# Kernel optimization log

Measured on AMD Instinct MI355X. Metric: run time of the kernel, lower is better.

## Reference

```python
import jax, jax.numpy as jnp
import numpy as np

B, S, DM, H, HD = 2, 4096, 768, 12, 64
SCALING = HD ** -0.5
LN_EPS = 1e-12
ROPE_BASE = 10000.0


def rotate_half(x):
    x1, x2 = jnp.split(x, 2, axis=-1)
    return jnp.concatenate([-x2, x1], axis=-1)


def setup_inputs() -> dict:
    key = jax.random.key(0)
    ks = jax.random.split(key, 8)
    s = 0.02
    hidden_states = jax.random.normal(ks[0], (B, S, DM), dtype=jnp.float32)
    # true rotary tables: inv_freq over head_dim/2, duplicated (HF convention)
    inv_freq = 1.0 / (ROPE_BASE ** (jnp.arange(0, HD, 2, dtype=jnp.float32) / HD))
    freqs = jnp.arange(S, dtype=jnp.float32)[:, None] * inv_freq[None, :]  # [S, HD/2]
    emb = jnp.concatenate([freqs, freqs], axis=-1)                          # [S, HD]
    cos, sin = jnp.cos(emb), jnp.sin(emb)
    return {
        "hidden_states": hidden_states,
        "cos": cos,
        "sin": sin,
        "Wq": jax.random.normal(ks[1], (DM, DM), dtype=jnp.float32) * s,
        "bq": jnp.zeros((DM,), dtype=jnp.float32),
        "Wk": jax.random.normal(ks[2], (DM, DM), dtype=jnp.float32) * s,
        "bk": jnp.zeros((DM,), dtype=jnp.float32),
        "Wv": jax.random.normal(ks[3], (DM, DM), dtype=jnp.float32) * s,
        "bv": jnp.zeros((DM,), dtype=jnp.float32),
        "Wo": jax.random.normal(ks[4], (DM, DM), dtype=jnp.float32) * s,
        "ln_g": jnp.ones((DM,), dtype=jnp.float32),
        "ln_b": jnp.zeros((DM,), dtype=jnp.float32),
    }


def reference(hidden_states, cos, sin, Wq, bq, Wk, bk, Wv, bv, Wo, ln_g, ln_b):
    # QKV projections -> [B, H, S, HD]
    def proj(W, b):
        return (hidden_states @ W.T + b).reshape(B, S, H, HD).transpose(0, 2, 1, 3)
    q, k, v = proj(Wq, bq), proj(Wk, bk), proj(Wv, bv)

    # RoPE (cos/sin broadcast over batch & heads)
    c = cos[None, None, :, :]
    s_ = sin[None, None, :, :]
    q = q * c + rotate_half(q) * s_
    k = k * c + rotate_half(k) * s_

    # Faithful to source: q pre-scaled, then eager attention scales scores again
    q = q * SCALING
    scores = jnp.einsum("bhsd,bhtd->bhst", q, k) * SCALING  # [B,H,S,S]
    probs = jax.nn.softmax(scores.astype(jnp.float32), axis=-1).astype(v.dtype)
    attn = jnp.einsum("bhst,bhtd->bhsd", probs, v)
    attn = attn.transpose(0, 2, 1, 3).reshape(B, S, DM)

    # output dense (no bias) + residual + LayerNorm
    out = attn @ Wo.T + hidden_states
    mu = jnp.mean(out, axis=-1, keepdims=True)
    var = jnp.var(out, axis=-1, keepdims=True)
    out = (out - mu) * jax.lax.rsqrt(var + LN_EPS) * ln_g + ln_b
    return out
```

## Files before the change

kernel.cpp:

```cpp
#include <hip/hip_runtime.h>
#include <math.h>

#define B_   2
#define S_   4096
#define DM_  768
#define H_   12
#define HD_  64
#define M_   (B_ * S_)
#define ROWELEMS ((size_t)M_ * DM_)
#define WELEMS  ((size_t)DM_ * DM_)

#define QSC (1.4426950408889634f / 64.0f)

typedef unsigned short u16;
typedef unsigned int   u32;
typedef __attribute__((ext_vector_type(8))) short  short8;
typedef __attribute__((ext_vector_type(4))) float  floatx4;

__device__ inline u16 f2bf(float f) {
    u32 u = __builtin_bit_cast(u32, f);
    u += 0x7FFF + ((u >> 16) & 1);
    return (u16)(u >> 16);
}
__device__ inline float bf2f(u16 h) {
    return __builtin_bit_cast(float, (u32)h << 16);
}
__device__ inline u32 pk_trunc(float a, float b) {
    return __builtin_amdgcn_perm(__builtin_bit_cast(u32, b),
                                 __builtin_bit_cast(u32, a), 0x07060302);
}

__device__ inline int sw_off(int r, int cg) {
    return (r << 6) + ((cg ^ (r & 7)) << 3);
}

__device__ __forceinline__ void load_lds16(const u16* g, u16* l) {
    __builtin_amdgcn_global_load_lds(
        (const __attribute__((address_space(1))) u32*)g,
        (__attribute__((address_space(3))) u32*)l, 16, 0, 0);
}

__global__ __launch_bounds__(256) void conv_bf16(
    const float* __restrict__ h,  const float* __restrict__ wq,
    const float* __restrict__ wk, const float* __restrict__ wv,
    const float* __restrict__ wo, u16* __restrict__ hb, u16* __restrict__ wb)
{
    const int y = blockIdx.y;
    const float* src; u16* dst; size_t n4;
    if (y == 0)      { src = h;  dst = hb;              n4 = ROWELEMS / 4; }
    else if (y == 1) { src = wq; dst = wb;              n4 = WELEMS / 4; }
    else if (y == 2) { src = wk; dst = wb + WELEMS;     n4 = WELEMS / 4; }
    else if (y == 3) { src = wv; dst = wb + 2 * WELEMS; n4 = WELEMS / 4; }
    else             { src = wo; dst = wb + 3 * WELEMS; n4 = WELEMS / 4; }
    const size_t stride = (size_t)gridDim.x * 256;
    for (size_t i = blockIdx.x * 256 + threadIdx.x; i < n4; i += stride) {
        float4 v = *(const float4*)&src[i * 4];
        u32 p0 = (u32)f2bf(v.x) | ((u32)f2bf(v.y) << 16);
        u32 p1 = (u32)f2bf(v.z) | ((u32)f2bf(v.w) << 16);
        *(uint2*)&dst[i * 4] = make_uint2(p0, p1);
    }
}

__global__ __launch_bounds__(256, 3) void gemm_qkv(
    const u16* __restrict__ A,
    const u16* __restrict__ W0, const u16* __restrict__ W1, const u16* __restrict__ W2,
    const float* __restrict__ b0, const float* __restrict__ b1, const float* __restrict__ b2,
    const float* __restrict__ cosT, const float* __restrict__ sinT,
    u16* __restrict__ Qh, u16* __restrict__ Kh, u16* __restrict__ Vt)
{
    __shared__ __align__(16) u16 As[128 * 64];
    __shared__ __align__(16) u16 Ws[128 * 64];

    const int tid  = threadIdx.x;
    const int wave = tid >> 6, lane = tid & 63;
    const int n16  = lane & 15, quad = lane >> 4;
    const int wm   = wave >> 1, wn = wave & 1;
    const int m0   = blockIdx.y * 128, n0 = blockIdx.x * 128;
    const int z    = blockIdx.z;

    const u16* Wz = (z == 0) ? W0 : (z == 1) ? W1 : W2;
    const float* bz = (z == 0) ? b0 : (z == 1) ? b1 : b2;

    int gao[4], ldso[4];
#pragma unroll
    for (int i = 0; i < 4; i++) {
        int g = wave * 256 + i * 64 + lane;
        int r = g >> 3, cg = (g & 7) ^ (r & 7);
        gao[i]  = r * DM_ + cg * 8;
        ldso[i] = (wave * 256 + i * 64) * 8;
    }
    const u16* Ap = A  + (size_t)m0 * DM_;
    const u16* Wp = Wz + (size_t)n0 * DM_;

    floatx4 acc[4][4];
#pragma unroll
    for (int i = 0; i < 4; i++)
#pragma unroll
        for (int j = 0; j < 4; j++) acc[i][j] = (floatx4){0.f, 0.f, 0.f, 0.f};

    for (int k0 = 0; k0 < DM_; k0 += 64) {
        __syncthreads();
#pragma unroll
        for (int i = 0; i < 4; i++) {
            load_lds16(Ap + k0 + gao[i], &As[ldso[i]]);
            load_lds16(Wp + k0 + gao[i], &Ws[ldso[i]]);
        }
        __syncthreads();
#pragma unroll
        for (int ks = 0; ks < 2; ks++) {
            short8 af[4], bf[4];
#pragma unroll
            for (int t = 0; t < 4; t++) {
                af[t] = *(const short8*)&As[sw_off(wm * 64 + t * 16 + n16, ks * 4 + quad)];
                bf[t] = *(const short8*)&Ws[sw_off(wn * 64 + t * 16 + n16, ks * 4 + quad)];
            }
#pragma unroll
            for (int i = 0; i < 4; i++)
#pragma unroll
                for (int j = 0; j < 4; j++)
                    acc[i][j] = __builtin_amdgcn_mfma_f32_16x16x32_bf16(
                        af[i], bf[j], acc[i][j], 0, 0, 0);
        }
    }

    if (z == 2) {
#pragma unroll
        for (int i = 0; i < 4; i++)
#pragma unroll
            for (int j = 0; j < 4; j++) {
                const int col = n0 + wn * 64 + j * 16 + n16;
                const int h = col >> 6, hd = col & 63;
                const int row0 = m0 + wm * 64 + i * 16 + quad * 4;
                const int b = row0 >> 12, s0 = row0 & 4095;
                const float bias = bz[col];
                float v0 = acc[i][j][0] + bias, v1 = acc[i][j][1] + bias;
                float v2 = acc[i][j][2] + bias, v3 = acc[i][j][3] + bias;
                u32 w0 = (u32)f2bf(v0) | ((u32)f2bf(v1) << 16);
                u32 w1 = (u32)f2bf(v2) | ((u32)f2bf(v3) << 16);
                *(uint2*)&Vt[((size_t)(b * H_ + h) * HD_ + hd) * S_ + s0] = make_uint2(w0, w1);
            }
    } else {
        u16* Out = (z == 0) ? Qh : Kh;
        const float sc_ = (z == 0) ? QSC : 1.0f;
#pragma unroll
        for (int i = 0; i < 4; i++)
#pragma unroll
            for (int j = 0; j < 2; j++) {
                const int col1 = n0 + wn * 64 + j * 16 + n16;
                const int col2 = col1 + 32;
                const int h = col1 >> 6, hd1 = col1 & 63;
                const float bias1 = bz[col1], bias2 = bz[col2];
#pragma unroll
                for (int r = 0; r < 4; r++) {
                    const int row = m0 + wm * 64 + i * 16 + quad * 4 + r;
                    const int b = row >> 12, s = row & 4095;
                    const float c  = cosT[s * HD_ + hd1];
                    const float sn = sinT[s * HD_ + hd1];
                    const float x1 = acc[i][j][r] + bias1;
                    const float x2 = acc[i][j + 2][r] + bias2;
                    u16* dst = Out + ((size_t)(b * H_ + h) * S_ + s) * HD_;
                    dst[hd1]      = f2bf((x1 * c - x2 * sn) * sc_);
                    dst[hd1 + 32] = f2bf((x2 * c + x1 * sn) * sc_);
                }
            }
    }
}

__global__ __launch_bounds__(256, 4) void flash_mfma(
    const u16* __restrict__ Qh, const u16* __restrict__ Kh,
    const u16* __restrict__ Vt, u16* __restrict__ O1, u16* __restrict__ O2,
    float* __restrict__ l1, float* __restrict__ l2)
{
    __shared__ __align__(16) u16 Ks[64 * 64];
    __shared__ __align__(16) u16 Vs[64 * 64];
    __shared__ __align__(16) u16 Ps[128 * 64];

    const int tid  = threadIdx.x;
    const int wave = tid >> 6, lane = tid & 63;
    const int n16  = lane & 15, quad = lane >> 4;
    const int qt   = blockIdx.x;
    const int bh   = blockIdx.y;
    const int z    = blockIdx.z;
    const size_t qk_base = (size_t)bh * S_ * HD_;
    const size_t vt_base = (size_t)bh * HD_ * S_;
    const int q0   = qt * 128;
    const int wrow = wave * 32;

    short8 qf[2][2];
#pragma unroll
    for (int rt = 0; rt < 2; rt++)
#pragma unroll
        for (int ks = 0; ks < 2; ks++)
            qf[rt][ks] = *(const short8*)&Qh[qk_base +
                (size_t)(q0 + wrow + rt * 16 + n16) * HD_ + ks * 32 + quad * 8];

    int gk_off[2], gv_off[2], ldso[2];
#pragma unroll
    for (int i = 0; i < 2; i++) {
        int g = wave * 128 + i * 64 + lane;
        int r = g >> 3, cg = (g & 7) ^ (r & 7);
        gk_off[i] = r * HD_ + cg * 8;
        gv_off[i] = r * S_  + cg * 8;
        ldso[i]   = (wave * 128 + i * 64) * 8;
    }

    floatx4 o_acc[2][4];
    float l_part[2] = {0.0f, 0.0f};
#pragma unroll
    for (int rt = 0; rt < 2; rt++)
#pragma unroll
        for (int dt = 0; dt < 4; dt++) o_acc[rt][dt] = (floatx4){0.f, 0.f, 0.f, 0.f};

    const u16* Kg = Kh + qk_base + (size_t)(z * 32) * 64 * HD_;
    const u16* Vg = Vt + vt_base + (size_t)(z * 32) * 64;

    for (int kt = 0; kt < 32; kt++) {
        __syncthreads();
#pragma unroll
        for (int i = 0; i < 2; i++) {
            load_lds16(Kg + gk_off[i], &Ks[ldso[i]]);
            load_lds16(Vg + gv_off[i], &Vs[ldso[i]]);
        }
        __syncthreads();
        Kg += 64 * HD_;
        Vg += 64;

        floatx4 sct[4][2];
#pragma unroll
        for (int ct = 0; ct < 4; ct++)
#pragma unroll
            for (int rt = 0; rt < 2; rt++)
                sct[ct][rt] = (floatx4){0.f, 0.f, 0.f, 0.f};
#pragma unroll
        for (int ks = 0; ks < 2; ks++) {
            short8 kf[4];
#pragma unroll
            for (int ct = 0; ct < 4; ct++)
                kf[ct] = *(const short8*)&Ks[sw_off(ct * 16 + n16, ks * 4 + quad)];
#pragma unroll
            for (int ct = 0; ct < 4; ct++)
#pragma unroll
                for (int rt = 0; rt < 2; rt++)
                    sct[ct][rt] = __builtin_amdgcn_mfma_f32_16x16x32_bf16(
                        kf[ct], qf[rt][ks], sct[ct][rt], 0, 0, 0);
        }

#pragma unroll
        for (int rt = 0; rt < 2; rt++)
#pragma unroll
            for (int ct = 0; ct < 4; ct++) {
                float p0 = __builtin_amdgcn_exp2f(sct[ct][rt][0]);
                float p1 = __builtin_amdgcn_exp2f(sct[ct][rt][1]);
                float p2 = __builtin_amdgcn_exp2f(sct[ct][rt][2]);
                float p3 = __builtin_amdgcn_exp2f(sct[ct][rt][3]);
                l_part[rt] += (p0 + p1) + (p2 + p3);
                uint2 w = make_uint2(pk_trunc(p0, p1), pk_trunc(p2, p3));
                const int row = wrow + rt * 16 + n16;
                const int off = sw_off(row, ct * 2 + (quad >> 1)) + (quad & 1) * 4;
                *(uint2*)&Ps[off] = w;
            }

#pragma unroll
        for (int ks = 0; ks < 2; ks++) {
            short8 pa[2];
#pragma unroll
            for (int rt = 0; rt < 2; rt++)
                pa[rt] = *(const short8*)&Ps[sw_off(wrow + rt * 16 + n16, ks * 4 + quad)];
            short8 vb[4];
#pragma unroll
            for (int dt = 0; dt < 4; dt++)
                vb[dt] = *(const short8*)&Vs[sw_off(dt * 16 + n16, ks * 4 + quad)];
#pragma unroll
            for (int rt = 0; rt < 2; rt++)
#pragma unroll
                for (int dt = 0; dt < 4; dt++)
                    o_acc[rt][dt] = __builtin_amdgcn_mfma_f32_16x16x32_bf16(
                        pa[rt], vb[dt], o_acc[rt][dt], 0, 0, 0);
        }
    }

    float* lz = z ? l2 : l1;
#pragma unroll
    for (int rt = 0; rt < 2; rt++) {
        float v = l_part[rt];
        v += __shfl_xor(v, 16);
        v += __shfl_xor(v, 32);
        if (lane < 16)
            lz[(size_t)bh * S_ + q0 + wrow + rt * 16 + lane] = v;
    }
    const int b = bh / H_, h = bh % H_;
    u16* Oz = z ? O2 : O1;
#pragma unroll
    for (int rt = 0; rt < 2; rt++)
#pragma unroll
        for (int r = 0; r < 4; r++) {
            const int srow = q0 + wrow + rt * 16 + quad * 4 + r;
            u16* Orow = Oz + ((size_t)b * S_ + srow) * DM_ + h * HD_;
#pragma unroll
            for (int dt = 0; dt < 4; dt++)
                Orow[dt * 16 + n16] = f2bf(o_acc[rt][dt][r]);
        }
}

__global__ __launch_bounds__(256, 4) void gemm_out(
    const u16* __restrict__ O1, const u16* __restrict__ O2,
    const float* __restrict__ l1, const float* __restrict__ l2,
    const u16* __restrict__ W, const float* __restrict__ resid,
    float* __restrict__ Cf)
{
    __shared__ __align__(16) u16 As[64 * 64];
    __shared__ __align__(16) u16 Ws[128 * 64];

    const int tid  = threadIdx.x;
    const int wave = tid >> 6, lane = tid & 63;
    const int n16  = lane & 15, quad = lane >> 4;
    const int wm   = wave >> 1, wn = wave & 1;
    const int m0   = blockIdx.y * 64, n0 = blockIdx.x * 128;

    int gwo[4], ldswo[4];
#pragma unroll
    for (int i = 0; i < 4; i++) {
        int g = wave * 256 + i * 64 + lane;
        int r = g >> 3, cg = (g & 7) ^ (r & 7);
        gwo[i]   = r * DM_ + cg * 8;
        ldswo[i] = (wave * 256 + i * 64) * 8;
    }
    const u16* Wp = W + (size_t)n0 * DM_;

    floatx4 acc[2][4];
#pragma unroll
    for (int i = 0; i < 2; i++)
#pragma unroll
        for (int j = 0; j < 4; j++) acc[i][j] = (floatx4){0.f, 0.f, 0.f, 0.f};

    for (int k0 = 0; k0 < DM_; k0 += 64) {
        __syncthreads();
#pragma unroll
        for (int i = 0; i < 4; i++)
            load_lds16(Wp + k0 + gwo[i], &Ws[ldswo[i]]);

#pragma unroll
        for (int i = 0; i < 2; i++) {
            const int ga = tid + i * 256;
            const int ra = ga >> 3, cga = ga & 7;
            const int row = m0 + ra;
            const int col0 = k0 + cga * 8;
            const int b = row >> 12, s = row & 4095, h = col0 >> 6;
            const size_t lidx = ((size_t)(b * H_ + h)) * S_ + s;
            const float inv = __builtin_amdgcn_rcpf(l1[lidx] + l2[lidx]);
            const size_t go = (size_t)row * DM_ + col0;
            uint4 a = *(const uint4*)&O1[go];
            uint4 c = *(const uint4*)&O2[go];
            u32 res[4];
#pragma unroll
            for (int w = 0; w < 4; w++) {
                u32 ua = (&a.x)[w], uc = (&c.x)[w];
                float x0 = bf2f((u16)(ua & 0xFFFF)) + bf2f((u16)(uc & 0xFFFF));
                float x1 = bf2f((u16)(ua >> 16))    + bf2f((u16)(uc >> 16));
                res[w] = (u32)f2bf(x0 * inv) | ((u32)f2bf(x1 * inv) << 16);
            }
            *(uint4*)&As[sw_off(ra, cga)] = make_uint4(res[0], res[1], res[2], res[3]);
        }
        __syncthreads();

#pragma unroll
        for (int ks = 0; ks < 2; ks++) {
            short8 af[2], bf[4];
#pragma unroll
            for (int rt = 0; rt < 2; rt++)
                af[rt] = *(const short8*)&As[sw_off(wm * 32 + rt * 16 + n16, ks * 4 + quad)];
#pragma unroll
            for (int ct = 0; ct < 4; ct++)
                bf[ct] = *(const short8*)&Ws[sw_off(wn * 64 + ct * 16 + n16, ks * 4 + quad)];
#pragma unroll
            for (int rt = 0; rt < 2; rt++)
#pragma unroll
                for (int ct = 0; ct < 4; ct++)
                    acc[rt][ct] = __builtin_amdgcn_mfma_f32_16x16x32_bf16(
                        af[rt], bf[ct], acc[rt][ct], 0, 0, 0);
        }
    }

#pragma unroll
    for (int rt = 0; rt < 2; rt++)
#pragma unroll
        for (int ct = 0; ct < 4; ct++) {
            const int col = n0 + wn * 64 + ct * 16 + n16;
#pragma unroll
            for (int r = 0; r < 4; r++) {
                const int row = m0 + wm * 32 + rt * 16 + quad * 4 + r;
                Cf[(size_t)row * DM_ + col] = acc[rt][ct][r] + resid[(size_t)row * DM_ + col];
            }
        }
}

__global__ __launch_bounds__(256) void ln_kernel(
    float* __restrict__ io, const float* __restrict__ g, const float* __restrict__ bb)
{
    const int row = blockIdx.x, t = threadIdx.x;
    float* p = io + (size_t)row * DM_;
    float x[3];
    float sum = 0.0f, sq = 0.0f;
#pragma unroll
    for (int i = 0; i < 3; i++) {
        x[i] = p[t + i * 256];
        sum += x[i];
        sq  = fmaf(x[i], x[i], sq);
    }
#pragma unroll
    for (int off = 32; off >= 1; off >>= 1) {
        sum += __shfl_xor(sum, off);
        sq  += __shfl_xor(sq, off);
    }
    __shared__ float s1[4], s2[4];
    if ((t & 63) == 0) { s1[t >> 6] = sum; s2[t >> 6] = sq; }
    __syncthreads();
    sum = s1[0] + s1[1] + s1[2] + s1[3];
    sq  = s2[0] + s2[1] + s2[2] + s2[3];
    const float mu  = sum * (1.0f / 768.0f);
    const float var = sq * (1.0f / 768.0f) - mu * mu;
    const float rs  = rsqrtf(var + 1e-12f);
#pragma unroll
    for (int i = 0; i < 3; i++) {
        const int c = t + i * 256;
        p[c] = (x[i] - mu) * rs * g[c] + bb[c];
    }
}

extern "C" void kernel_launch(void* const* d_in, const int* in_sizes, int n_in,
                              void* d_out, int out_size, void* d_ws, size_t ws_size,
                              hipStream_t stream)
{
    const float* hidden = (const float*)d_in[0];
    const float* cosT   = (const float*)d_in[1];
    const float* sinT   = (const float*)d_in[2];
    const float* Wq     = (const float*)d_in[3];
    const float* bq     = (const float*)d_in[4];
    const float* Wk     = (const float*)d_in[5];
    const float* bk     = (const float*)d_in[6];
    const float* Wv     = (const float*)d_in[7];
    const float* bv     = (const float*)d_in[8];
    const float* Wo     = (const float*)d_in[9];
    const float* ln_g   = (const float*)d_in[10];
    const float* ln_b   = (const float*)d_in[11];
    float* out = (float*)d_out;

    u16* wsb = (u16*)d_ws;
    u16* Hb  = wsb;
    u16* Wb  = wsb + ROWELEMS;
    u16* Qh  = Wb + 4 * WELEMS;
    u16* Kh  = Qh + ROWELEMS;
    u16* Vt  = Kh + ROWELEMS;
    u16* O2  = Vt + ROWELEMS;
    float* l1 = (float*)(O2 + ROWELEMS);
    float* l2 = l1 + (size_t)B_ * H_ * S_;
    u16* O1  = Hb;
    u16* Wqb = Wb, *Wkb = Wb + WELEMS, *Wvb = Wb + 2 * WELEMS, *Wob = Wb + 3 * WELEMS;

    conv_bf16<<<dim3(1024, 5), 256, 0, stream>>>(hidden, Wq, Wk, Wv, Wo, Hb, Wb);

    gemm_qkv<<<dim3(DM_ / 128, M_ / 128, 3), 256, 0, stream>>>(
        Hb, Wqb, Wkb, Wvb, bq, bk, bv, cosT, sinT, Qh, Kh, Vt);

    flash_mfma<<<dim3(S_ / 128, B_ * H_, 2), 256, 0, stream>>>(
        Qh, Kh, Vt, O1, O2, l1, l2);

    gemm_out<<<dim3(DM_ / 128, M_ / 64), 256, 0, stream>>>(
        O1, O2, l1, l2, Wob, hidden, out);

    ln_kernel<<<M_, 256, 0, stream>>>(out, ln_g, ln_b);
}
```

Measured before the change: 300.9 us.

## Double-buffer K/V tiles in flash kernel and compute row sums via MFMA

The flash attention kernel now double-buffers K and V tiles in LDS. It prefetches the next tile while computing on the current one and drops one of the two barriers per iteration. The softmax denominator is now computed with an extra MFMA against a ones vector on the bf16-truncated probabilities, replacing the scalar accumulation and shuffle reduction. Launch bounds drop to 3 blocks per SM to fit the larger LDS footprint. The single barrier plus waitcnt ordering, and computing the sum from truncated P, could introduce races or small numeric differences.

```diff
diff --git a/kernel.cpp b/kernel.cpp
--- a/kernel.cpp
+++ b/kernel.cpp
@@ -166,13 +166,13 @@
     }
 }
 
-__global__ __launch_bounds__(256, 4) void flash_mfma(
+__global__ __launch_bounds__(256, 3) void flash_mfma(
     const u16* __restrict__ Qh, const u16* __restrict__ Kh,
     const u16* __restrict__ Vt, u16* __restrict__ O1, u16* __restrict__ O2,
     float* __restrict__ l1, float* __restrict__ l2)
 {
-    __shared__ __align__(16) u16 Ks[64 * 64];
-    __shared__ __align__(16) u16 Vs[64 * 64];
+    __shared__ __align__(16) u16 Ks[2][64 * 64];
+    __shared__ __align__(16) u16 Vs[2][64 * 64];
     __shared__ __align__(16) u16 Ps[128 * 64];
 
     const int tid  = threadIdx.x;
@@ -194,6 +194,10 @@
             qf[rt][ks] = *(const short8*)&Qh[qk_base +
                 (size_t)(q0 + wrow + rt * 16 + n16) * HD_ + ks * 32 + quad * 8];
 
+    short8 ones;
+#pragma unroll
+    for (int j = 0; j < 8; j++) ones[j] = (short)0x3F80;
+
     int gk_off[2], gv_off[2], ldso[2];
 #pragma unroll
     for (int i = 0; i < 2; i++) {
@@ -205,25 +209,38 @@
     }
 
     floatx4 o_acc[2][4];
-    float l_part[2] = {0.0f, 0.0f};
-#pragma unroll
-    for (int rt = 0; rt < 2; rt++)
+    floatx4 o_l[2];
+#pragma unroll
+    for (int rt = 0; rt < 2; rt++) {
+        o_l[rt] = (floatx4){0.f, 0.f, 0.f, 0.f};
 #pragma unroll
         for (int dt = 0; dt < 4; dt++) o_acc[rt][dt] = (floatx4){0.f, 0.f, 0.f, 0.f};
-
-    const u16* Kg = Kh + qk_base + (size_t)(z * 32) * 64 * HD_;
-    const u16* Vg = Vt + vt_base + (size_t)(z * 32) * 64;
+    }
+
+    const u16* Kg0 = Kh + qk_base + (size_t)(z * 32) * 64 * HD_;
+    const u16* Vg0 = Vt + vt_base + (size_t)(z * 32) * 64;
+
+#pragma unroll
+    for (int i = 0; i < 2; i++) {
+        load_lds16(Kg0 + gk_off[i], &Ks[0][ldso[i]]);
+        load_lds16(Vg0 + gv_off[i], &Vs[0][ldso[i]]);
+    }
 
     for (int kt = 0; kt < 32; kt++) {
+        const int cur = kt & 1, nxt = cur ^ 1;
         __syncthreads();
-#pragma unroll
-        for (int i = 0; i < 2; i++) {
-            load_lds16(Kg + gk_off[i], &Ks[ldso[i]]);
-            load_lds16(Vg + gv_off[i], &Vs[ldso[i]]);
-        }
-        __syncthreads();
-        Kg += 64 * HD_;
-        Vg += 64;
+
+        {
+            const int ktn = (kt < 31) ? kt + 1 : 31;
+            const u16* Kg = Kg0 + (size_t)ktn * 64 * HD_;
+            const u16* Vg = Vg0 + (size_t)ktn * 64;
+#pragma unroll
+            for (int i = 0; i < 2; i++) {
+                load_lds16(Kg + gk_off[i], &Ks[nxt][ldso[i]]);
+                load_lds16(Vg + gv_off[i], &Vs[nxt][ldso[i]]);
+            }
+        }
+        __builtin_amdgcn_s_waitcnt(0x0F74);
 
         floatx4 sct[4][2];
 #pragma unroll
@@ -236,7 +253,7 @@
             short8 kf[4];
 #pragma unroll
             for (int ct = 0; ct < 4; ct++)
-                kf[ct] = *(const short8*)&Ks[sw_off(ct * 16 + n16, ks * 4 + quad)];
+                kf[ct] = *(const short8*)&Ks[cur][sw_off(ct * 16 + n16, ks * 4 + quad)];
 #pragma unroll
             for (int ct = 0; ct < 4; ct++)
 #pragma unroll
@@ -253,7 +270,6 @@
                 float p1 = __builtin_amdgcn_exp2f(sct[ct][rt][1]);
                 float p2 = __builtin_amdgcn_exp2f(sct[ct][rt][2]);
                 float p3 = __builtin_amdgcn_exp2f(sct[ct][rt][3]);
-                l_part[rt] += (p0 + p1) + (p2 + p3);
                 uint2 w = make_uint2(pk_trunc(p0, p1), pk_trunc(p2, p3));
                 const int row = wrow + rt * 16 + n16;
                 const int off = sw_off(row, ct * 2 + (quad >> 1)) + (quad & 1) * 4;
@@ -269,24 +285,26 @@
             short8 vb[4];
 #pragma unroll
             for (int dt = 0; dt < 4; dt++)
-                vb[dt] = *(const short8*)&Vs[sw_off(dt * 16 + n16, ks * 4 + quad)];
-#pragma unroll
-            for (int rt = 0; rt < 2; rt++)
+                vb[dt] = *(const short8*)&Vs[cur][sw_off(dt * 16 + n16, ks * 4 + quad)];
+#pragma unroll
+            for (int rt = 0; rt < 2; rt++) {
 #pragma unroll
                 for (int dt = 0; dt < 4; dt++)
                     o_acc[rt][dt] = __builtin_amdgcn_mfma_f32_16x16x32_bf16(
                         pa[rt], vb[dt], o_acc[rt][dt], 0, 0, 0);
+                o_l[rt] = __builtin_amdgcn_mfma_f32_16x16x32_bf16(
+                    pa[rt], ones, o_l[rt], 0, 0, 0);
+            }
         }
     }
 
     float* lz = z ? l2 : l1;
-#pragma unroll
-    for (int rt = 0; rt < 2; rt++) {
-        float v = l_part[rt];
-        v += __shfl_xor(v, 16);
-        v += __shfl_xor(v, 32);
-        if (lane < 16)
-            lz[(size_t)bh * S_ + q0 + wrow + rt * 16 + lane] = v;
+    if (n16 == 0) {
+#pragma unroll
+        for (int rt = 0; rt < 2; rt++)
+#pragma unroll
+            for (int r = 0; r < 4; r++)
+                lz[(size_t)bh * S_ + q0 + wrow + rt * 16 + quad * 4 + r] = o_l[rt][r];
     }
     const int b = bh / H_, h = bh % H_;
     u16* Oz = z ? O2 : O1;
```

Result: no change. 299.0 us (-0.6%).

## Double query rows per flash block to reuse K/V tiles across more rows

Applied to the files above, without the earlier changes.

Each flash attention block now covers 256 query rows instead of 128, with each wave owning 64 rows, so every K/V tile staged in shared memory serves twice as many queries. QK^T and the exp/pack step are restructured to loop per 16-row tile, with K fragments loaded once per tile, which keeps the live score registers small. The aim is to halve global K/V traffic and the number of syncthreads per unit of work. In exchange, register and LDS use per block go up (launch bounds drop to 3 blocks per CU) and the grid halves to 768 blocks.

```diff
diff --git a/kernel.cpp b/kernel.cpp
--- a/kernel.cpp
+++ b/kernel.cpp
@@ -166,14 +166,14 @@
     }
 }
 
-__global__ __launch_bounds__(256, 4) void flash_mfma(
+__global__ __launch_bounds__(256, 3) void flash_mfma(
     const u16* __restrict__ Qh, const u16* __restrict__ Kh,
     const u16* __restrict__ Vt, u16* __restrict__ O1, u16* __restrict__ O2,
     float* __restrict__ l1, float* __restrict__ l2)
 {
     __shared__ __align__(16) u16 Ks[64 * 64];
     __shared__ __align__(16) u16 Vs[64 * 64];
-    __shared__ __align__(16) u16 Ps[128 * 64];
+    __shared__ __align__(16) u16 Ps[256 * 64];
 
     const int tid  = threadIdx.x;
     const int wave = tid >> 6, lane = tid & 63;
@@ -183,12 +183,12 @@
     const int z    = blockIdx.z;
     const size_t qk_base = (size_t)bh * S_ * HD_;
     const size_t vt_base = (size_t)bh * HD_ * S_;
-    const int q0   = qt * 128;
-    const int wrow = wave * 32;
-
-    short8 qf[2][2];
-#pragma unroll
-    for (int rt = 0; rt < 2; rt++)
+    const int q0   = qt * 256;
+    const int wrow = wave * 64;
+
+    short8 qf[4][2];
+#pragma unroll
+    for (int rt = 0; rt < 4; rt++)
 #pragma unroll
         for (int ks = 0; ks < 2; ks++)
             qf[rt][ks] = *(const short8*)&Qh[qk_base +
@@ -204,84 +204,79 @@
         ldso[i]   = (wave * 128 + i * 64) * 8;
     }
 
-    floatx4 o_acc[2][4];
-    float l_part[2] = {0.0f, 0.0f};
-#pragma unroll
-    for (int rt = 0; rt < 2; rt++)
+    floatx4 o_acc[4][4];
+    float l_part[4] = {0.f, 0.f, 0.f, 0.f};
+#pragma unroll
+    for (int rt = 0; rt < 4; rt++)
 #pragma unroll
         for (int dt = 0; dt < 4; dt++) o_acc[rt][dt] = (floatx4){0.f, 0.f, 0.f, 0.f};
 
-    const u16* Kg = Kh + qk_base + (size_t)(z * 32) * 64 * HD_;
-    const u16* Vg = Vt + vt_base + (size_t)(z * 32) * 64;
+    const u16* Kg0 = Kh + qk_base + (size_t)(z * 32) * 64 * HD_;
+    const u16* Vg0 = Vt + vt_base + (size_t)(z * 32) * 64;
 
     for (int kt = 0; kt < 32; kt++) {
         __syncthreads();
 #pragma unroll
         for (int i = 0; i < 2; i++) {
-            load_lds16(Kg + gk_off[i], &Ks[ldso[i]]);
-            load_lds16(Vg + gv_off[i], &Vs[ldso[i]]);
-        }
-        __syncthreads();
-        Kg += 64 * HD_;
-        Vg += 64;
-
-        floatx4 sct[4][2];
-#pragma unroll
-        for (int ct = 0; ct < 4; ct++)
-#pragma unroll
-            for (int rt = 0; rt < 2; rt++)
-                sct[ct][rt] = (floatx4){0.f, 0.f, 0.f, 0.f};
+            load_lds16(Kg0 + (size_t)kt * 64 * HD_ + gk_off[i], &Ks[ldso[i]]);
+            load_lds16(Vg0 + (size_t)kt * 64       + gv_off[i], &Vs[ldso[i]]);
+        }
+        __syncthreads();
+
+        {
+            short8 kf[2][4];
+#pragma unroll
+            for (int ks = 0; ks < 2; ks++)
+#pragma unroll
+                for (int ct = 0; ct < 4; ct++)
+                    kf[ks][ct] = *(const short8*)&Ks[sw_off(ct * 16 + n16, ks * 4 + quad)];
+
+#pragma unroll
+            for (int rt = 0; rt < 4; rt++) {
+                floatx4 sct[4];
+#pragma unroll
+                for (int ct = 0; ct < 4; ct++) sct[ct] = (floatx4){0.f, 0.f, 0.f, 0.f};
+#pragma unroll
+                for (int ks = 0; ks < 2; ks++)
+#pragma unroll
+                    for (int ct = 0; ct < 4; ct++)
+                        sct[ct] = __builtin_amdgcn_mfma_f32_16x16x32_bf16(
+                            kf[ks][ct], qf[rt][ks], sct[ct], 0, 0, 0);
+                const int row = wrow + rt * 16 + n16;
+#pragma unroll
+                for (int ct = 0; ct < 4; ct++) {
+                    float p0 = __builtin_amdgcn_exp2f(sct[ct][0]);
+                    float p1 = __builtin_amdgcn_exp2f(sct[ct][1]);
+                    float p2 = __builtin_amdgcn_exp2f(sct[ct][2]);
+                    float p3 = __builtin_amdgcn_exp2f(sct[ct][3]);
+                    l_part[rt] += (p0 + p1) + (p2 + p3);
+                    uint2 w = make_uint2(pk_trunc(p0, p1), pk_trunc(p2, p3));
+                    const int off = sw_off(row, ct * 2 + (quad >> 1)) + (quad & 1) * 4;
+                    *(uint2*)&Ps[off] = w;
+                }
+            }
+        }
+
 #pragma unroll
         for (int ks = 0; ks < 2; ks++) {
-            short8 kf[4];
-#pragma unroll
-            for (int ct = 0; ct < 4; ct++)
-                kf[ct] = *(const short8*)&Ks[sw_off(ct * 16 + n16, ks * 4 + quad)];
-#pragma unroll
-            for (int ct = 0; ct < 4; ct++)
-#pragma unroll
-                for (int rt = 0; rt < 2; rt++)
-                    sct[ct][rt] = __builtin_amdgcn_mfma_f32_16x16x32_bf16(
-                        kf[ct], qf[rt][ks], sct[ct][rt], 0, 0, 0);
-        }
-
-#pragma unroll
-        for (int rt = 0; rt < 2; rt++)
-#pragma unroll
-            for (int ct = 0; ct < 4; ct++) {
-                float p0 = __builtin_amdgcn_exp2f(sct[ct][rt][0]);
-                float p1 = __builtin_amdgcn_exp2f(sct[ct][rt][1]);
-                float p2 = __builtin_amdgcn_exp2f(sct[ct][rt][2]);
-                float p3 = __builtin_amdgcn_exp2f(sct[ct][rt][3]);
-                l_part[rt] += (p0 + p1) + (p2 + p3);
-                uint2 w = make_uint2(pk_trunc(p0, p1), pk_trunc(p2, p3));
-                const int row = wrow + rt * 16 + n16;
-                const int off = sw_off(row, ct * 2 + (quad >> 1)) + (quad & 1) * 4;
-                *(uint2*)&Ps[off] = w;
-            }
-
-#pragma unroll
-        for (int ks = 0; ks < 2; ks++) {
-            short8 pa[2];
-#pragma unroll
-            for (int rt = 0; rt < 2; rt++)
-                pa[rt] = *(const short8*)&Ps[sw_off(wrow + rt * 16 + n16, ks * 4 + quad)];
             short8 vb[4];
 #pragma unroll
             for (int dt = 0; dt < 4; dt++)
                 vb[dt] = *(const short8*)&Vs[sw_off(dt * 16 + n16, ks * 4 + quad)];
 #pragma unroll
-            for (int rt = 0; rt < 2; rt++)
+            for (int rt = 0; rt < 4; rt++) {
+                short8 pa = *(const short8*)&Ps[sw_off(wrow + rt * 16 + n16, ks * 4 + quad)];
 #pragma unroll
                 for (int dt = 0; dt < 4; dt++)
                     o_acc[rt][dt] = __builtin_amdgcn_mfma_f32_16x16x32_bf16(
-                        pa[rt], vb[dt], o_acc[rt][dt], 0, 0, 0);
+                        pa, vb[dt], o_acc[rt][dt], 0, 0, 0);
+            }
         }
     }
 
     float* lz = z ? l2 : l1;
 #pragma unroll
-    for (int rt = 0; rt < 2; rt++) {
+    for (int rt = 0; rt < 4; rt++) {
         float v = l_part[rt];
         v += __shfl_xor(v, 16);
         v += __shfl_xor(v, 32);
@@ -291,7 +286,7 @@
     const int b = bh / H_, h = bh % H_;
     u16* Oz = z ? O2 : O1;
 #pragma unroll
-    for (int rt = 0; rt < 2; rt++)
+    for (int rt = 0; rt < 4; rt++)
 #pragma unroll
         for (int r = 0; r < 4; r++) {
             const int srow = q0 + wrow + rt * 16 + quad * 4 + r;
@@ -462,7 +457,7 @@
     gemm_qkv<<<dim3(DM_ / 128, M_ / 128, 3), 256, 0, stream>>>(
         Hb, Wqb, Wkb, Wvb, bq, bk, bv, cosT, sinT, Qh, Kh, Vt);
 
-    flash_mfma<<<dim3(S_ / 128, B_ * H_, 2), 256, 0, stream>>>(
+    flash_mfma<<<dim3(S_ / 256, B_ * H_, 2), 256, 0, stream>>>(
         Qh, Kh, Vt, O1, O2, l1, l2);
 
     gemm_out<<<dim3(DM_ / 128, M_ / 64), 256, 0, stream>>>(
```

New measurement: 417.9 us. 38.9% more time.
